# Kernel optimization log

Hardware: AMD Instinct MI355X
Metric: run time of the kernel (lower is better)

The kernel has to match this reference:

```python
import jax, jax.numpy as jnp
import numpy as np

B, N, C, G, H, DK = 8, 128, 128, 2, 4, 32
BN_SCALE = float(1.0 / np.sqrt(1.0 + 1e-5))  # eval-mode BatchNorm with running_mean=0, var=1, gamma=1, beta=0


def _l1norm(x):
    # F.normalize(p=1, dim=-1)
    return x / jnp.maximum(jnp.sum(jnp.abs(x), -1, keepdims=True), 1e-12)


def _bn(x):
    return x * BN_SCALE


def _lrelu(x):
    return jax.nn.leaky_relu(x, 0.01)


def setup_inputs() -> dict:
    key = jax.random.key(0)
    ks = jax.random.split(key, 14)
    p = lambda i, shape: jax.random.normal(ks[i], shape, jnp.float32) * 0.05
    return {
        "vp": jax.random.normal(ks[0], (B, N, C), jnp.float32),
        "ep0": jax.random.uniform(ks[1], (B, N, N), jnp.float32),
        # PointSimilarity_Pre 1x1-conv stack (stored as [in, out] matrices)
        "ps_pre_w1": p(2, (C, 2 * C)), "ps_pre_w2": p(3, (2 * C, C)),
        "ps_pre_w3": p(4, (C, 1)), "ps_pre_b3": jnp.zeros((1,), jnp.float32),
        # Per-generation PointSimilarity2 stacks
        "ps_w1": p(5, (G, C, 2 * C)), "ps_w2": p(6, (G, 2 * C, C)),
        "ps_w3": p(7, (G, C, 1)), "ps_b3": jnp.zeros((G, 1), jnp.float32),
        # Per-generation D2PAgg stacks (input is cat(vp, aggr) -> 2C channels)
        "d2p_w1": p(8, (G, 2 * C, 2 * C)), "d2p_w2": p(9, (G, 2 * C, C)),
        # Per-generation multi-head attention projections (d_model=C, n_head*d_k=C)
        "mha_wq": p(10, (G, C, H * DK)), "mha_wk": p(11, (G, C, H * DK)),
    }


def _psim(vp, ep_last, w1, w2, w3, b3, kval):
    # pairwise l2 distance features: [B, N, N, C]
    sim = (vp[:, :, None, :] - vp[:, None, :, :]) ** 2
    h = _lrelu(_bn(jnp.einsum('bijc,co->bijo', sim, w1)))
    h = _lrelu(_bn(jnp.einsum('bijc,co->bijo', h, w2)))
    e = jax.nn.sigmoid(jnp.einsum('bijc,co->bijo', h, w3)[..., 0] + b3)
    eye = jnp.eye(vp.shape[1], dtype=vp.dtype)
    ep_last = ep_last * (1.0 - eye)
    ep_sum = jnp.sum(ep_last, -1, keepdims=True)
    e = e * ep_last
    if kval is not None:  # neighbor attention via top-k sparsification
        _, idx = jax.lax.top_k(e, kval)
        b_i = jnp.arange(e.shape[0])[:, None, None]
        r_i = jnp.arange(e.shape[1])[None, :, None]
        mask = jnp.zeros_like(e).at[b_i, r_i, idx].set(1.0)
        e = e * mask
    e = _l1norm(e) * ep_sum
    e = e + eye + 1e-6
    e = e / jnp.sum(e, 2, keepdims=True)
    return e


def _d2p(ep, vp, w1, w2):
    eye = jnp.eye(vp.shape[1], dtype=vp.dtype)
    edge = _l1norm(ep * (1.0 - eye))
    aggr = jnp.einsum('bij,bjc->bic', edge, vp)  # bmm aggregation
    nf = jnp.concatenate([vp, aggr], -1)         # [B, N, 2C]
    h = _lrelu(_bn(nf @ w1))
    return _lrelu(_bn(h @ w2))


def _mha(vp, wq, wk):
    b, n, _ = vp.shape
    q = (vp @ wq).reshape(b, n, H, DK)
    k = (vp @ wk).reshape(b, n, H, DK)
    attn = jax.nn.softmax(jnp.einsum('bqhd,bkhd->bhqk', q, k) / np.sqrt(DK), axis=-1)
    return attn.mean(1)  # average heads -> [B, N, N]


def reference(vp, ep0, ps_pre_w1, ps_pre_w2, ps_pre_w3, ps_pre_b3,
              ps_w1, ps_w2, ps_w3, ps_b3, d2p_w1, d2p_w2, mha_wq, mha_wk):
    ep = _psim(vp, ep0, ps_pre_w1, ps_pre_w2, ps_pre_w3, ps_pre_b3, None)
    for g in range(G):
        attn = _mha(vp, mha_wq[g], mha_wk[g])
        vp = _d2p(ep * attn, vp, d2p_w1[g], d2p_w2[g])
        kval = int(N * (1.0 - 0.1 * (g + 1)))
        ep = _psim(vp, ep, ps_w1[g], ps_w2[g], ps_w3[g], ps_b3[g], kval)
    return ep
```

## Files before the change

### kernel.cpp

```cpp
#include <hip/hip_runtime.h>

typedef __bf16 bf16x8 __attribute__((ext_vector_type(8)));
typedef float floatx4 __attribute__((ext_vector_type(4)));

#define MFMA(a, b, c) __builtin_amdgcn_mfma_f32_16x16x32_bf16(a, b, c, 0, 0, 0)

#define BNS 0.9999950000374997f
#define LRELU(x) ((x) > 0.f ? (x) : 0.01f * (x))

__device__ inline float wave_sum(float v) {
#pragma unroll
  for (int s = 32; s > 0; s >>= 1) v += __shfl_xor(v, s, 64);
  return v;
}
__device__ inline float wave_max(float v) {
#pragma unroll
  for (int s = 32; s > 0; s >>= 1) v = fmaxf(v, __shfl_xor(v, s, 64));
  return v;
}

__global__ __launch_bounds__(256) void k_prep(const float* __restrict__ pre_w1,
                                              const float* __restrict__ ps_w1,
                                              const float* __restrict__ pre_w2,
                                              const float* __restrict__ ps_w2,
                                              const float* __restrict__ dw1,
                                              const float* __restrict__ dw2,
                                              const float* __restrict__ mwq,
                                              const float* __restrict__ mwk,
                                              __bf16* __restrict__ w1b,
                                              __bf16* __restrict__ w2b,
                                              __bf16* __restrict__ d1i,
                                              __bf16* __restrict__ d2i,
                                              __bf16* __restrict__ qki) {
  const int tt = blockIdx.x * 256 + threadIdx.x;
  bf16x8 v;
  if (tt < 24576) {
    const int buf = tt / 12288;
    const int r = tt % 12288;
    const int set = r >> 12;
    const int q = r & 4095;
    const int ln = q & 63, qd = ln >> 4, cc = ln & 15;
    const int wv = (q >> 6) & 3;
    if (buf == 0) {
      const int kt = (q >> 8) & 3, qtr = (q >> 10) & 3;
      const float* src = (set == 0) ? pre_w1 : ps_w1 + (size_t)(set - 1) * 32768;
      const float* p = src + (size_t)(kt * 32 + qd * 8) * 256 + qtr * 64 + wv * 16 + cc;
#pragma unroll
      for (int jj = 0; jj < 8; jj++) v[jj] = (__bf16)p[jj * 256];
      *(bf16x8*)&w1b[(size_t)set * 32768 + q * 8] = v;
    } else {
      const int kt = (q >> 8) & 1, nt = (q >> 9) & 1, qtr = (q >> 10) & 3;
      const float* src = (set == 0) ? pre_w2 : ps_w2 + (size_t)(set - 1) * 32768;
      const float* p = src + (size_t)(qtr * 64 + kt * 32 + qd * 8) * 128 + wv * 32 + nt * 16 + cc;
#pragma unroll
      for (int jj = 0; jj < 8; jj++) v[jj] = (__bf16)p[jj * 128];
      *(bf16x8*)&w2b[(size_t)set * 32768 + q * 8] = v;
    }
  } else if (tt < 40960) {
    const int u = tt - 24576;
    const int gen = u >> 13, r = u & 8191, cb = r >> 8, o = r & 255;
    const float* src = dw1 + (size_t)gen * 65536 + (size_t)(cb * 8) * 256 + o;
#pragma unroll
    for (int jj = 0; jj < 8; jj++) v[jj] = (__bf16)src[jj * 256];
    *(bf16x8*)&d1i[(size_t)(((gen * 32 + cb) * 256 + o)) * 8] = v;
  } else if (tt < 49152) {
    const int u = tt - 40960;
    const int gen = u >> 12, r = u & 4095, kb = r >> 7, o = r & 127;
    const float* src = dw2 + (size_t)gen * 32768 + (size_t)(kb * 8) * 128 + o;
#pragma unroll
    for (int jj = 0; jj < 8; jj++) v[jj] = (__bf16)src[jj * 128];
    *(bf16x8*)&d2i[(size_t)(((gen * 32 + kb) * 128 + o)) * 8] = v;
  } else if (tt < 57344) {
    const int u = tt - 49152;
    const int gen = u >> 12, r = u & 4095, qk = r >> 11, r2 = r & 2047;
    const int cb = r2 >> 7, o = r2 & 127;
    const float* src = (qk ? mwk : mwq) + (size_t)gen * 16384 + (size_t)(cb * 8) * 128 + o;
#pragma unroll
    for (int jj = 0; jj < 8; jj++) v[jj] = (__bf16)src[jj * 128];
    *(bf16x8*)&qki[(size_t)((((gen * 2 + qk) * 16 + cb) * 128 + o)) * 8] = v;
  }
}

__global__ void __launch_bounds__(256, 3)
k_psim(const float* __restrict__ vp, const float* __restrict__ ep_in,
       float* __restrict__ ep_out,
       const __bf16* __restrict__ w1b, const __bf16* __restrict__ w2b,
       const float* __restrict__ w3, const float* __restrict__ b3,
       int kval, float* __restrict__ outp) {
  __shared__ __bf16 simf[16384];
  __shared__ __bf16 hbf[8192];
  __shared__ float ep_row[128];
  __shared__ float e_row[128];
  __shared__ float w3s[128];
  __shared__ float red[256];
  __shared__ float red2[4];

  const int tid = threadIdx.x;
  const int b = blockIdx.x >> 7, i = blockIdx.x & 127;
  const float* vpb = vp + ((size_t)b << 14);
  const float* vpi = vpb + (i << 7);
  const size_t rowoff = ((size_t)blockIdx.x) << 7;

  {
    const int j = tid >> 1;
    const int c0 = (tid & 1) << 6;
    const int m = j >> 4, ccr = j & 15;
    const float* vpj = vpb + (j << 7) + c0;
    const float* vpx = vpi + c0;
#pragma unroll
    for (int c = 0; c < 64; c += 8) {
      const int gc = c0 + c;
      const int kt = gc >> 5, qdw = (gc >> 3) & 3;
      float4 a0 = *(const float4*)(vpj + c);
      float4 a1 = *(const float4*)(vpj + c + 4);
      float4 b0 = *(const float4*)(vpx + c);
      float4 b1 = *(const float4*)(vpx + c + 4);
      bf16x8 t;
      float d;
      d = a0.x - b0.x; t[0] = (__bf16)(d * d);
      d = a0.y - b0.y; t[1] = (__bf16)(d * d);
      d = a0.z - b0.z; t[2] = (__bf16)(d * d);
      d = a0.w - b0.w; t[3] = (__bf16)(d * d);
      d = a1.x - b1.x; t[4] = (__bf16)(d * d);
      d = a1.y - b1.y; t[5] = (__bf16)(d * d);
      d = a1.z - b1.z; t[6] = (__bf16)(d * d);
      d = a1.w - b1.w; t[7] = (__bf16)(d * d);
      *(bf16x8*)&simf[(((kt << 3) + m) << 6 | (qdw << 4 | ccr)) << 3] = t;
    }
    if (tid < 128) {
      ep_row[tid] = (tid == i) ? 0.f : ep_in[rowoff + tid];
      w3s[tid] = w3[tid];
    }
  }
  __syncthreads();

  const int wv = tid >> 6;
  const int ln = tid & 63;
  const int qd = ln >> 4;
  const int cc = ln & 15;

  floatx4 acc2[8][2];
#pragma unroll
  for (int m = 0; m < 8; m++) {
    acc2[m][0] = (floatx4){0.f, 0.f, 0.f, 0.f};
    acc2[m][1] = (floatx4){0.f, 0.f, 0.f, 0.f};
  }

  const int h1h = wv >> 1;
  const int h1qd = ((wv & 1) << 1) | (cc >> 3);
  const int h1jj = cc & 7;

  for (int qtr = 0; qtr < 4; qtr++) {
    bf16x8 bw[4];
#pragma unroll
    for (int kt = 0; kt < 4; kt++)
      bw[kt] = *(const bf16x8*)&w1b[((((qtr * 4 + kt) * 4 + wv) * 64) + ln) * 8];
#pragma unroll
    for (int m2 = 0; m2 < 8; m2 += 2) {
      bf16x8 af0[4], af1[4];
#pragma unroll
      for (int kt = 0; kt < 4; kt++) {
        af0[kt] = *(const bf16x8*)&simf[(((kt << 3) + m2) << 6 | ln) << 3];
        af1[kt] = *(const bf16x8*)&simf[(((kt << 3) + m2 + 1) << 6 | ln) << 3];
      }
      floatx4 x0 = (floatx4){0.f, 0.f, 0.f, 0.f};
      floatx4 x1 = (floatx4){0.f, 0.f, 0.f, 0.f};
#pragma unroll
      for (int kt = 0; kt < 4; kt++) {
        x0 = MFMA(af0[kt], bw[kt], x0);
        x1 = MFMA(af1[kt], bw[kt], x1);
      }
#pragma unroll
      for (int r = 0; r < 4; r++) {
        float v0 = x0[r] * BNS;
        float v1 = x1[r] * BNS;
        hbf[(((h1h * 8 + m2) * 64) + h1qd * 16 + qd * 4 + r) * 8 + h1jj] = (__bf16)LRELU(v0);
        hbf[(((h1h * 8 + m2 + 1) * 64) + h1qd * 16 + qd * 4 + r) * 8 + h1jj] = (__bf16)LRELU(v1);
      }
    }
    __syncthreads();

    bf16x8 bw2[2][2];
#pragma unroll
    for (int nt = 0; nt < 2; nt++)
#pragma unroll
      for (int kt = 0; kt < 2; kt++)
        bw2[nt][kt] = *(const bf16x8*)&w2b[(((((qtr * 2 + nt) * 2 + kt) * 4 + wv) * 64) + ln) * 8];
#pragma unroll
    for (int m = 0; m < 8; m++) {
      bf16x8 a0 = *(const bf16x8*)&hbf[((m << 6) | ln) << 3];
      bf16x8 a1 = *(const bf16x8*)&hbf[(((8 + m) << 6) | ln) << 3];
      acc2[m][0] = MFMA(a0, bw2[0][0], acc2[m][0]);
      acc2[m][1] = MFMA(a0, bw2[1][0], acc2[m][1]);
      acc2[m][0] = MFMA(a1, bw2[0][1], acc2[m][0]);
      acc2[m][1] = MFMA(a1, bw2[1][1], acc2[m][1]);
    }
    __syncthreads();
  }

  {
    const int seg = wv;
#pragma unroll
    for (int m = 0; m < 8; m++)
#pragma unroll
      for (int nt = 0; nt < 2; nt++) {
        const int q2 = (nt << 1) | (cc >> 3);
#pragma unroll
        for (int r = 0; r < 4; r++) {
          float v = acc2[m][nt][r] * BNS;
          simf[(((seg * 8 + m) * 64) + q2 * 16 + qd * 4 + r) * 8 + (cc & 7)] = (__bf16)LRELU(v);
        }
      }
  }
  __syncthreads();

  {
    const int j = tid & 127, hh = tid >> 7;
    const int m = j >> 4, R = j & 15;
    float s = 0.f;
#pragma unroll
    for (int sg = 0; sg < 2; sg++) {
      const int seg = hh * 2 + sg;
#pragma unroll
      for (int q3 = 0; q3 < 4; q3++) {
        bf16x8 f = *(const bf16x8*)&simf[(((seg * 8 + m) * 64) + q3 * 16 + R) * 8];
        const float* wp = &w3s[seg * 32 + q3 * 8];
#pragma unroll
        for (int jj = 0; jj < 8; jj++) s += (float)f[jj] * wp[jj];
      }
    }
    red[tid] = s;
  }
  __syncthreads();
  if (tid < 128) {
    float s = red[tid] + red[tid + 128] + b3[0];
    float sg = 1.f / (1.f + expf(-s));
    e_row[tid] = sg * ep_row[tid];
  }
  __syncthreads();

  {
    float v = (tid < 128) ? ep_row[tid] : 0.f;
    float w = wave_sum(v);
    if (ln == 0) red2[wv] = w;
  }
  __syncthreads();
  const float ep_sum = red2[0] + red2[1];

  if (kval > 0) {
    const int j = tid & 127, hh = tid >> 7;
    const float v = e_row[j];
    int cnt = 0;
    const int base = hh << 6;
#pragma unroll 8
    for (int jj = 0; jj < 64; jj++) {
      float u = e_row[base + jj];
      cnt += (u > v || (u == v && (base + jj) < j)) ? 1 : 0;
    }
    red[tid] = (float)cnt;
  }
  __syncthreads();

  float em = 0.f;
  if (tid < 128) {
    float v = e_row[tid];
    if (kval > 0) {
      int cnt = (int)red[tid] + (int)red[tid + 128];
      em = (cnt < kval) ? v : 0.f;
    } else {
      em = v;
    }
  }
  {
    float w = wave_sum((tid < 128) ? em : 0.f);
    if (ln == 0) red2[wv] = w;
  }
  __syncthreads();
  const float l1 = red2[0] + red2[1];
  __syncthreads();

  const float scale = ep_sum / fmaxf(l1, 1e-12f);
  float val = 0.f;
  if (tid < 128) val = em * scale + ((tid == i) ? 1.f : 0.f) + 1e-6f;
  {
    float w = wave_sum((tid < 128) ? val : 0.f);
    if (ln == 0) red2[wv] = w;
  }
  __syncthreads();
  const float rsum = red2[0] + red2[1];

  if (tid < 128) {
    float o = val / rsum;
    ep_out[rowoff + tid] = o;
    if (outp) outp[rowoff + tid] = o;
  }
}

__global__ __launch_bounds__(256) void k_qk(const float* __restrict__ vp,
                                            const __bf16* __restrict__ qkw,
                                            float* __restrict__ qo,
                                            float* __restrict__ ko) {
  __shared__ float vr[128];
  const int t = threadIdx.x;
  const size_t rowoff = ((size_t)blockIdx.x) << 7;
  if (t < 128) vr[t] = vp[rowoff + t];
  __syncthreads();
  const int o = t & 127;
  const __bf16* base = qkw + ((t >> 7) ? 16384 : 0);
  const float4* vr4 = (const float4*)vr;
  float a = 0.f;
#pragma unroll
  for (int cb = 0; cb < 16; cb++) {
    bf16x8 w8 = *(const bf16x8*)&base[(cb * 128 + o) * 8];
    float4 v0 = vr4[2 * cb], v1 = vr4[2 * cb + 1];
    a += v0.x * (float)w8[0] + v0.y * (float)w8[1] + v0.z * (float)w8[2] + v0.w * (float)w8[3] +
         v1.x * (float)w8[4] + v1.y * (float)w8[5] + v1.z * (float)w8[6] + v1.w * (float)w8[7];
  }
  float* dst = (t < 128) ? qo : ko;
  dst[rowoff + o] = a;
}

__global__ __launch_bounds__(256) void k_attn_d2p(const float* __restrict__ qv,
                                                  const float* __restrict__ kv,
                                                  const float* __restrict__ ep,
                                                  const float* __restrict__ vp_in,
                                                  const __bf16* __restrict__ d1,
                                                  const __bf16* __restrict__ d2,
                                                  float* __restrict__ vp_out) {
  __shared__ float qi[256];
  __shared__ float sbuf[1024];
  __shared__ float er[256];
  __shared__ float nf[512];
  __shared__ float hb[512];
  __shared__ float pbuf[2048];
  __shared__ float red2[4];

  const int tid = threadIdx.x;
  const int wv = tid >> 6, ln = tid & 63;
  const int b = blockIdx.x >> 6;
  const int r0 = (blockIdx.x & 63) * 2;
  const size_t rowoff0 = ((size_t)(b * 128 + r0)) << 7;
  const float* vpbb = vp_in + ((size_t)b << 14);

  qi[tid] = qv[rowoff0 + tid];
  __syncthreads();

  {
    const int j = tid & 127, hh = tid >> 7;
    const float* krow = kv + (((size_t)(b * 128 + j)) << 7);
    const int h0 = hh * 2, h1 = hh * 2 + 1;
    float s00 = 0.f, s01 = 0.f, s10 = 0.f, s11 = 0.f;
#pragma unroll
    for (int d = 0; d < 32; d += 4) {
      float4 k0 = *(const float4*)(krow + h0 * 32 + d);
      float4 k1 = *(const float4*)(krow + h1 * 32 + d);
      s00 += qi[h0 * 32 + d] * k0.x + qi[h0 * 32 + d + 1] * k0.y +
             qi[h0 * 32 + d + 2] * k0.z + qi[h0 * 32 + d + 3] * k0.w;
      s01 += qi[h1 * 32 + d] * k1.x + qi[h1 * 32 + d + 1] * k1.y +
             qi[h1 * 32 + d + 2] * k1.z + qi[h1 * 32 + d + 3] * k1.w;
      s10 += qi[128 + h0 * 32 + d] * k0.x + qi[128 + h0 * 32 + d + 1] * k0.y +
             qi[128 + h0 * 32 + d + 2] * k0.z + qi[128 + h0 * 32 + d + 3] * k0.w;
      s11 += qi[128 + h1 * 32 + d] * k1.x + qi[128 + h1 * 32 + d + 1] * k1.y +
             qi[128 + h1 * 32 + d + 2] * k1.z + qi[128 + h1 * 32 + d + 3] * k1.w;
    }
    const float sc = 0.17677669529663687f;
    sbuf[(0 * 4 + h0) * 128 + j] = s00 * sc;
    sbuf[(0 * 4 + h1) * 128 + j] = s01 * sc;
    sbuf[(1 * 4 + h0) * 128 + j] = s10 * sc;
    sbuf[(1 * 4 + h1) * 128 + j] = s11 * sc;
  }
  __syncthreads();

  {
    const int g = wv;
#pragma unroll
    for (int row = 0; row < 2; row++) {
      float a = sbuf[(row * 4 + g) * 128 + ln];
      float bb = sbuf[(row * 4 + g) * 128 + 64 + ln];
      float mx = wave_max(fmaxf(a, bb));
      float e0 = expf(a - mx), e1 = expf(bb - mx);
      float Z = wave_sum(e0 + e1);
      sbuf[(row * 4 + g) * 128 + ln] = e0 / Z;
      sbuf[(row * 4 + g) * 128 + 64 + ln] = e1 / Z;
    }
  }
  __syncthreads();

  {
    const int row = tid >> 7, j = tid & 127;
    float attn = 0.25f * (sbuf[(row * 4) * 128 + j] + sbuf[(row * 4 + 1) * 128 + j] +
                          sbuf[(row * 4 + 2) * 128 + j] + sbuf[(row * 4 + 3) * 128 + j]);
    float eraw = (j == r0 + row) ? 0.f : ep[rowoff0 + tid] * attn;
    float w = wave_sum(eraw);
    if (ln == 0) red2[wv] = w;
    __syncthreads();
    float l1row = red2[row * 2] + red2[row * 2 + 1];
    er[tid] = eraw / fmaxf(l1row, 1e-12f);
    nf[(row << 8) + j] = vp_in[rowoff0 + tid];
  }
  __syncthreads();

  {
    const int cg = tid & 31, jg = tid >> 5;
    float4 a0 = {0.f, 0.f, 0.f, 0.f}, a1 = {0.f, 0.f, 0.f, 0.f};
#pragma unroll
    for (int jj = 0; jj < 16; jj++) {
      const int j = jg * 16 + jj;
      float4 v = *(const float4*)(vpbb + (j << 7) + (cg << 2));
      float e0 = er[j], e1 = er[128 + j];
      a0.x += e0 * v.x; a0.y += e0 * v.y; a0.z += e0 * v.z; a0.w += e0 * v.w;
      a1.x += e1 * v.x; a1.y += e1 * v.y; a1.z += e1 * v.z; a1.w += e1 * v.w;
    }
    *(float4*)&pbuf[(jg * 32 + cg) * 4] = a0;
    *(float4*)&pbuf[1024 + (jg * 32 + cg) * 4] = a1;
  }
  __syncthreads();
  {
    const int row = tid >> 7, c = tid & 127;
    float s = 0.f;
#pragma unroll
    for (int jg = 0; jg < 8; jg++) s += pbuf[(row << 10) + jg * 128 + c];
    nf[(row << 8) + 128 + c] = s;
  }
  __syncthreads();

  {
    const int row = tid >> 7, o = tid & 127;
    const float4* nfr4 = (const float4*)&nf[row << 8];
    float a0 = 0.f, a1 = 0.f;
#pragma unroll 4
    for (int cb = 0; cb < 32; cb++) {
      bf16x8 wa = *(const bf16x8*)&d1[(cb * 256 + o) * 8];
      bf16x8 wb = *(const bf16x8*)&d1[(cb * 256 + o + 128) * 8];
      float4 n0 = nfr4[2 * cb], n1 = nfr4[2 * cb + 1];
      a0 += n0.x * (float)wa[0] + n0.y * (float)wa[1] + n0.z * (float)wa[2] + n0.w * (float)wa[3] +
            n1.x * (float)wa[4] + n1.y * (float)wa[5] + n1.z * (float)wa[6] + n1.w * (float)wa[7];
      a1 += n0.x * (float)wb[0] + n0.y * (float)wb[1] + n0.z * (float)wb[2] + n0.w * (float)wb[3] +
            n1.x * (float)wb[4] + n1.y * (float)wb[5] + n1.z * (float)wb[6] + n1.w * (float)wb[7];
    }
    hb[(row << 8) + o] = LRELU(a0 * BNS);
    hb[(row << 8) + o + 128] = LRELU(a1 * BNS);
  }
  __syncthreads();

  {
    const int row = tid >> 7, o = tid & 127;
    const float4* hbr4 = (const float4*)&hb[row << 8];
    float a = 0.f;
#pragma unroll 4
    for (int kb = 0; kb < 32; kb++) {
      bf16x8 w8 = *(const bf16x8*)&d2[(kb * 128 + o) * 8];
      float4 h0 = hbr4[2 * kb], h1 = hbr4[2 * kb + 1];
      a += h0.x * (float)w8[0] + h0.y * (float)w8[1] + h0.z * (float)w8[2] + h0.w * (float)w8[3] +
           h1.x * (float)w8[4] + h1.y * (float)w8[5] + h1.z * (float)w8[6] + h1.w * (float)w8[7];
    }
    vp_out[rowoff0 + tid] = LRELU(a * BNS);
  }
}

extern "C" void kernel_launch(void* const* d_in, const int* in_sizes, int n_in,
                              void* d_out, int out_size, void* d_ws, size_t ws_size,
                              hipStream_t stream) {
  const float* vp0    = (const float*)d_in[0];
  const float* ep0    = (const float*)d_in[1];
  const float* pre_w1 = (const float*)d_in[2];
  const float* pre_w2 = (const float*)d_in[3];
  const float* pre_w3 = (const float*)d_in[4];
  const float* pre_b3 = (const float*)d_in[5];
  const float* ps_w1  = (const float*)d_in[6];
  const float* ps_w2  = (const float*)d_in[7];
  const float* ps_w3  = (const float*)d_in[8];
  const float* ps_b3  = (const float*)d_in[9];
  const float* dw1    = (const float*)d_in[10];
  const float* dw2    = (const float*)d_in[11];
  const float* mwq    = (const float*)d_in[12];
  const float* mwk    = (const float*)d_in[13];

  char* ws = (char*)d_ws;
  float* ep   = (float*)(ws);
  float* vpb  = (float*)(ws + (512ull << 10));
  float* vpa  = (float*)(ws + (1024ull << 10));
  float* qf   = (float*)(ws + (1536ull << 10));
  float* kf   = (float*)(ws + (2048ull << 10));
  __bf16* w1b = (__bf16*)(ws + (2560ull << 10));
  __bf16* w2b = (__bf16*)(ws + (2560ull << 10) + 196608);
  __bf16* d1i = (__bf16*)(ws + (2560ull << 10) + 393216);
  __bf16* d2i = (__bf16*)(ws + (2560ull << 10) + 655360);
  __bf16* qki = (__bf16*)(ws + (2560ull << 10) + 786432);
  float* outp = (float*)d_out;

  k_prep<<<224, 256, 0, stream>>>(pre_w1, ps_w1, pre_w2, ps_w2, dw1, dw2, mwq, mwk,
                                  w1b, w2b, d1i, d2i, qki);

  k_psim<<<1024, 256, 0, stream>>>(vp0, ep0, ep, w1b, w2b, pre_w3, pre_b3, 0, nullptr);

  k_qk<<<1024, 256, 0, stream>>>(vp0, qki, qf, kf);
  k_attn_d2p<<<512, 256, 0, stream>>>(qf, kf, ep, vp0, d1i, d2i, vpb);
  k_psim<<<1024, 256, 0, stream>>>(vpb, ep, ep, w1b + 32768, w2b + 32768,
                                   ps_w3, ps_b3, 115, nullptr);

  k_qk<<<1024, 256, 0, stream>>>(vpb, qki + 32768, qf, kf);
  k_attn_d2p<<<512, 256, 0, stream>>>(qf, kf, ep, vpb, d1i + 65536, d2i + 32768, vpa);
  k_psim<<<1024, 256, 0, stream>>>(vpa, ep, ep, w1b + 65536, w2b + 65536,
                                   ps_w3 + 128, ps_b3 + 1, 102, outp);
}
```

Baseline: 231.3 us.

## Partition psim MLP by rows per wave, keeping features in registers

Restructures the pairwise-similarity MLP so each wave owns 32 neighbor rows and computes all output channels for them. The squared-difference features are built directly in registers, which removes the shared simf buffer. Per-wave hbf slices replace block-wide barriers inside the qtr loop. The final w3 projection is done from the accumulators with lane shuffles instead of a shared-memory round trip. This cuts LDS traffic and __syncthreads, at the cost of each wave loading all of w1/w2 and holding more accumulator registers, and the prep kernel's weight layouts are reordered to match.

```diff
diff --git a/kernel.cpp b/kernel.cpp
--- a/kernel.cpp
+++ b/kernel.cpp
@@ -40,18 +40,17 @@
     const int set = r >> 12;
     const int q = r & 4095;
     const int ln = q & 63, qd = ln >> 4, cc = ln & 15;
-    const int wv = (q >> 6) & 3;
     if (buf == 0) {
-      const int kt = (q >> 8) & 3, qtr = (q >> 10) & 3;
+      const int kt = (q >> 6) & 3, nt = (q >> 8) & 3, qtr = q >> 10;
       const float* src = (set == 0) ? pre_w1 : ps_w1 + (size_t)(set - 1) * 32768;
-      const float* p = src + (size_t)(kt * 32 + qd * 8) * 256 + qtr * 64 + wv * 16 + cc;
+      const float* p = src + (size_t)(kt * 32 + qd * 8) * 256 + qtr * 64 + nt * 16 + cc;
 #pragma unroll
       for (int jj = 0; jj < 8; jj++) v[jj] = (__bf16)p[jj * 256];
       *(bf16x8*)&w1b[(size_t)set * 32768 + q * 8] = v;
     } else {
-      const int kt = (q >> 8) & 1, nt = (q >> 9) & 1, qtr = (q >> 10) & 3;
+      const int kt = (q >> 6) & 1, ot = (q >> 7) & 7, qtr = q >> 10;
       const float* src = (set == 0) ? pre_w2 : ps_w2 + (size_t)(set - 1) * 32768;
-      const float* p = src + (size_t)(qtr * 64 + kt * 32 + qd * 8) * 128 + wv * 32 + nt * 16 + cc;
+      const float* p = src + (size_t)(qtr * 64 + kt * 32 + qd * 8) * 128 + ot * 16 + cc;
 #pragma unroll
       for (int jj = 0; jj < 8; jj++) v[jj] = (__bf16)p[jj * 128];
       *(bf16x8*)&w2b[(size_t)set * 32768 + q * 8] = v;
@@ -87,34 +86,39 @@
        const __bf16* __restrict__ w1b, const __bf16* __restrict__ w2b,
        const float* __restrict__ w3, const float* __restrict__ b3,
        int kval, float* __restrict__ outp) {
-  __shared__ __bf16 simf[16384];
   __shared__ __bf16 hbf[8192];
   __shared__ float ep_row[128];
   __shared__ float e_row[128];
+  __shared__ float pre_s[128];
   __shared__ float w3s[128];
   __shared__ float red[256];
   __shared__ float red2[4];
 
   const int tid = threadIdx.x;
+  const int wv = tid >> 6, ln = tid & 63;
+  const int qd = ln >> 4, cc = ln & 15;
   const int b = blockIdx.x >> 7, i = blockIdx.x & 127;
   const float* vpb = vp + ((size_t)b << 14);
   const float* vpi = vpb + (i << 7);
   const size_t rowoff = ((size_t)blockIdx.x) << 7;
 
-  {
-    const int j = tid >> 1;
-    const int c0 = (tid & 1) << 6;
-    const int m = j >> 4, ccr = j & 15;
-    const float* vpj = vpb + (j << 7) + c0;
-    const float* vpx = vpi + c0;
-#pragma unroll
-    for (int c = 0; c < 64; c += 8) {
-      const int gc = c0 + c;
-      const int kt = gc >> 5, qdw = (gc >> 3) & 3;
-      float4 a0 = *(const float4*)(vpj + c);
-      float4 a1 = *(const float4*)(vpj + c + 4);
-      float4 b0 = *(const float4*)(vpx + c);
-      float4 b1 = *(const float4*)(vpx + c + 4);
+  if (tid < 128) {
+    ep_row[tid] = (tid == i) ? 0.f : ep_in[rowoff + tid];
+    w3s[tid] = w3[tid];
+  }
+
+  bf16x8 af[2][4];
+#pragma unroll
+  for (int m2 = 0; m2 < 2; m2++) {
+    const int j = wv * 32 + m2 * 16 + cc;
+    const float* vpj = vpb + (j << 7);
+#pragma unroll
+    for (int kt = 0; kt < 4; kt++) {
+      const int c0 = kt * 32 + qd * 8;
+      float4 a0 = *(const float4*)(vpj + c0);
+      float4 a1 = *(const float4*)(vpj + c0 + 4);
+      float4 b0 = *(const float4*)(vpi + c0);
+      float4 b1 = *(const float4*)(vpi + c0 + 4);
       bf16x8 t;
       float d;
       d = a0.x - b0.x; t[0] = (__bf16)(d * d);
@@ -125,115 +129,80 @@
       d = a1.y - b1.y; t[5] = (__bf16)(d * d);
       d = a1.z - b1.z; t[6] = (__bf16)(d * d);
       d = a1.w - b1.w; t[7] = (__bf16)(d * d);
-      *(bf16x8*)&simf[(((kt << 3) + m) << 6 | (qdw << 4 | ccr)) << 3] = t;
-    }
-    if (tid < 128) {
-      ep_row[tid] = (tid == i) ? 0.f : ep_in[rowoff + tid];
-      w3s[tid] = w3[tid];
-    }
-  }
-  __syncthreads();
-
-  const int wv = tid >> 6;
-  const int ln = tid & 63;
-  const int qd = ln >> 4;
-  const int cc = ln & 15;
-
-  floatx4 acc2[8][2];
-#pragma unroll
-  for (int m = 0; m < 8; m++) {
-    acc2[m][0] = (floatx4){0.f, 0.f, 0.f, 0.f};
-    acc2[m][1] = (floatx4){0.f, 0.f, 0.f, 0.f};
-  }
-
-  const int h1h = wv >> 1;
-  const int h1qd = ((wv & 1) << 1) | (cc >> 3);
-  const int h1jj = cc & 7;
+      af[m2][kt] = t;
+    }
+  }
+
+  floatx4 acc2[2][8];
+#pragma unroll
+  for (int m2 = 0; m2 < 2; m2++)
+#pragma unroll
+    for (int ot = 0; ot < 8; ot++) acc2[m2][ot] = (floatx4){0.f, 0.f, 0.f, 0.f};
+
+  const int hbase = wv * 2048;
+  const int jj_s = cc & 7;
 
   for (int qtr = 0; qtr < 4; qtr++) {
-    bf16x8 bw[4];
-#pragma unroll
-    for (int kt = 0; kt < 4; kt++)
-      bw[kt] = *(const bf16x8*)&w1b[((((qtr * 4 + kt) * 4 + wv) * 64) + ln) * 8];
-#pragma unroll
-    for (int m2 = 0; m2 < 8; m2 += 2) {
-      bf16x8 af0[4], af1[4];
-#pragma unroll
-      for (int kt = 0; kt < 4; kt++) {
-        af0[kt] = *(const bf16x8*)&simf[(((kt << 3) + m2) << 6 | ln) << 3];
-        af1[kt] = *(const bf16x8*)&simf[(((kt << 3) + m2 + 1) << 6 | ln) << 3];
-      }
-      floatx4 x0 = (floatx4){0.f, 0.f, 0.f, 0.f};
-      floatx4 x1 = (floatx4){0.f, 0.f, 0.f, 0.f};
-#pragma unroll
-      for (int kt = 0; kt < 4; kt++) {
-        x0 = MFMA(af0[kt], bw[kt], x0);
-        x1 = MFMA(af1[kt], bw[kt], x1);
-      }
-#pragma unroll
-      for (int r = 0; r < 4; r++) {
-        float v0 = x0[r] * BNS;
-        float v1 = x1[r] * BNS;
-        hbf[(((h1h * 8 + m2) * 64) + h1qd * 16 + qd * 4 + r) * 8 + h1jj] = (__bf16)LRELU(v0);
-        hbf[(((h1h * 8 + m2 + 1) * 64) + h1qd * 16 + qd * 4 + r) * 8 + h1jj] = (__bf16)LRELU(v1);
-      }
-    }
-    __syncthreads();
-
-    bf16x8 bw2[2][2];
-#pragma unroll
-    for (int nt = 0; nt < 2; nt++)
-#pragma unroll
-      for (int kt = 0; kt < 2; kt++)
-        bw2[nt][kt] = *(const bf16x8*)&w2b[(((((qtr * 2 + nt) * 2 + kt) * 4 + wv) * 64) + ln) * 8];
-#pragma unroll
-    for (int m = 0; m < 8; m++) {
-      bf16x8 a0 = *(const bf16x8*)&hbf[((m << 6) | ln) << 3];
-      bf16x8 a1 = *(const bf16x8*)&hbf[(((8 + m) << 6) | ln) << 3];
-      acc2[m][0] = MFMA(a0, bw2[0][0], acc2[m][0]);
-      acc2[m][1] = MFMA(a0, bw2[1][0], acc2[m][1]);
-      acc2[m][0] = MFMA(a1, bw2[0][1], acc2[m][0]);
-      acc2[m][1] = MFMA(a1, bw2[1][1], acc2[m][1]);
-    }
-    __syncthreads();
-  }
-
-  {
-    const int seg = wv;
-#pragma unroll
-    for (int m = 0; m < 8; m++)
-#pragma unroll
-      for (int nt = 0; nt < 2; nt++) {
-        const int q2 = (nt << 1) | (cc >> 3);
+#pragma unroll
+    for (int nt = 0; nt < 4; nt++) {
+      bf16x8 bw[4];
+#pragma unroll
+      for (int kt = 0; kt < 4; kt++)
+        bw[kt] = *(const bf16x8*)&w1b[(size_t)(((qtr * 4 + nt) * 4 + kt) * 64 + ln) * 8];
+      const int kt2 = nt >> 1;
+      const int qd2 = ((nt << 1) | (cc >> 3)) & 3;
+#pragma unroll
+      for (int m2 = 0; m2 < 2; m2++) {
+        floatx4 x = (floatx4){0.f, 0.f, 0.f, 0.f};
+#pragma unroll
+        for (int kt = 0; kt < 4; kt++) x = MFMA(af[m2][kt], bw[kt], x);
+        const int base = hbase + ((kt2 * 2 + m2) * 64 + qd2 * 16) * 8 + jj_s;
 #pragma unroll
         for (int r = 0; r < 4; r++) {
-          float v = acc2[m][nt][r] * BNS;
-          simf[(((seg * 8 + m) * 64) + q2 * 16 + qd * 4 + r) * 8 + (cc & 7)] = (__bf16)LRELU(v);
+          float v = x[r] * BNS;
+          hbf[base + (qd * 4 + r) * 8] = (__bf16)LRELU(v);
         }
       }
-  }
-  __syncthreads();
-
-  {
-    const int j = tid & 127, hh = tid >> 7;
-    const int m = j >> 4, R = j & 15;
-    float s = 0.f;
-#pragma unroll
-    for (int sg = 0; sg < 2; sg++) {
-      const int seg = hh * 2 + sg;
-#pragma unroll
-      for (int q3 = 0; q3 < 4; q3++) {
-        bf16x8 f = *(const bf16x8*)&simf[(((seg * 8 + m) * 64) + q3 * 16 + R) * 8];
-        const float* wp = &w3s[seg * 32 + q3 * 8];
-#pragma unroll
-        for (int jj = 0; jj < 8; jj++) s += (float)f[jj] * wp[jj];
+    }
+    bf16x8 a2[2][2];
+#pragma unroll
+    for (int m2 = 0; m2 < 2; m2++)
+#pragma unroll
+      for (int kt = 0; kt < 2; kt++)
+        a2[m2][kt] = *(const bf16x8*)&hbf[hbase + ((kt * 2 + m2) * 64 + ln) * 8];
+#pragma unroll
+    for (int ot = 0; ot < 8; ot++) {
+      bf16x8 bo0 = *(const bf16x8*)&w2b[(size_t)(((qtr * 8 + ot) * 2 + 0) * 64 + ln) * 8];
+      bf16x8 bo1 = *(const bf16x8*)&w2b[(size_t)(((qtr * 8 + ot) * 2 + 1) * 64 + ln) * 8];
+#pragma unroll
+      for (int m2 = 0; m2 < 2; m2++) {
+        acc2[m2][ot] = MFMA(a2[m2][0], bo0, acc2[m2][ot]);
+        acc2[m2][ot] = MFMA(a2[m2][1], bo1, acc2[m2][ot]);
       }
     }
-    red[tid] = s;
+  }
+
+  __syncthreads();
+
+#pragma unroll
+  for (int m2 = 0; m2 < 2; m2++) {
+#pragma unroll
+    for (int r = 0; r < 4; r++) {
+      float p = 0.f;
+#pragma unroll
+      for (int ot = 0; ot < 8; ot++) {
+        float h = acc2[m2][ot][r] * BNS;
+        h = LRELU(h);
+        p += h * w3s[ot * 16 + cc];
+      }
+#pragma unroll
+      for (int mk = 1; mk < 16; mk <<= 1) p += __shfl_xor(p, mk, 64);
+      if (cc == 0) pre_s[wv * 32 + m2 * 16 + qd * 4 + r] = p;
+    }
   }
   __syncthreads();
   if (tid < 128) {
-    float s = red[tid] + red[tid + 128] + b3[0];
+    float s = pre_s[tid] + b3[0];
     float sg = 1.f / (1.f + expf(-s));
     e_row[tid] = sg * ep_row[tid];
   }
```

Result: slower. 242.1 us (+4.7%).

## Prefetch psim MFMA weights one quarter ahead and use one row per attn_d2p block

Applied to the files above, without the earlier changes.

In k_psim the bf16 weight fragments for the two MFMA stages are loaded one quarter-iteration ahead into registers, and the quarter loop is fully unrolled. This hides global weight-load latency behind the MFMA work. k_attn_d2p now handles one query row per block instead of two, launching 1024 blocks, which doubles parallelism and shrinks shared memory. The cost is extra register pressure in psim and more redundant reads of d1/d2 weights, since each block now covers half as many rows, and some threads sit idle in the reworked attention kernel.

```diff
diff --git a/kernel.cpp b/kernel.cpp
--- a/kernel.cpp
+++ b/kernel.cpp
@@ -101,6 +101,11 @@
   const float* vpi = vpb + (i << 7);
   const size_t rowoff = ((size_t)blockIdx.x) << 7;
 
+  const int wv = tid >> 6;
+  const int ln = tid & 63;
+  const int qd = ln >> 4;
+  const int cc = ln & 15;
+
   {
     const int j = tid >> 1;
     const int c0 = (tid & 1) << 6;
@@ -132,12 +137,18 @@
       w3s[tid] = w3[tid];
     }
   }
-  __syncthreads();
-
-  const int wv = tid >> 6;
-  const int ln = tid & 63;
-  const int qd = ln >> 4;
-  const int cc = ln & 15;
+
+  bf16x8 bw[4], bw2[2][2];
+#pragma unroll
+  for (int kt = 0; kt < 4; kt++)
+    bw[kt] = *(const bf16x8*)&w1b[(((0 * 4 + kt) * 4 + wv) * 64 + ln) * 8];
+#pragma unroll
+  for (int nt = 0; nt < 2; nt++)
+#pragma unroll
+    for (int kt = 0; kt < 2; kt++)
+      bw2[nt][kt] = *(const bf16x8*)&w2b[((((0 * 2 + nt) * 2 + kt) * 4 + wv) * 64 + ln) * 8];
+
+  __syncthreads();
 
   floatx4 acc2[8][2];
 #pragma unroll
@@ -150,11 +161,20 @@
   const int h1qd = ((wv & 1) << 1) | (cc >> 3);
   const int h1jj = cc & 7;
 
+#pragma unroll
   for (int qtr = 0; qtr < 4; qtr++) {
-    bf16x8 bw[4];
-#pragma unroll
-    for (int kt = 0; kt < 4; kt++)
-      bw[kt] = *(const bf16x8*)&w1b[((((qtr * 4 + kt) * 4 + wv) * 64) + ln) * 8];
+    bf16x8 bwn[4], bw2n[2][2];
+    if (qtr < 3) {
+#pragma unroll
+      for (int kt = 0; kt < 4; kt++)
+        bwn[kt] = *(const bf16x8*)&w1b[((((qtr + 1) * 4 + kt) * 4 + wv) * 64 + ln) * 8];
+#pragma unroll
+      for (int nt = 0; nt < 2; nt++)
+#pragma unroll
+        for (int kt = 0; kt < 2; kt++)
+          bw2n[nt][kt] = *(const bf16x8*)&w2b[(((((qtr + 1) * 2 + nt) * 2 + kt) * 4 + wv) * 64 + ln) * 8];
+    }
+
 #pragma unroll
     for (int m2 = 0; m2 < 8; m2 += 2) {
       bf16x8 af0[4], af1[4];
@@ -180,12 +200,6 @@
     }
     __syncthreads();
 
-    bf16x8 bw2[2][2];
-#pragma unroll
-    for (int nt = 0; nt < 2; nt++)
-#pragma unroll
-      for (int kt = 0; kt < 2; kt++)
-        bw2[nt][kt] = *(const bf16x8*)&w2b[(((((qtr * 2 + nt) * 2 + kt) * 4 + wv) * 64) + ln) * 8];
 #pragma unroll
     for (int m = 0; m < 8; m++) {
       bf16x8 a0 = *(const bf16x8*)&hbf[((m << 6) | ln) << 3];
@@ -196,6 +210,15 @@
       acc2[m][1] = MFMA(a1, bw2[1][1], acc2[m][1]);
     }
     __syncthreads();
+
+    if (qtr < 3) {
+#pragma unroll
+      for (int kt = 0; kt < 4; kt++) bw[kt] = bwn[kt];
+#pragma unroll
+      for (int nt = 0; nt < 2; nt++)
+#pragma unroll
+        for (int kt = 0; kt < 2; kt++) bw2[nt][kt] = bw2n[nt][kt];
+    }
   }
 
   {
@@ -327,125 +350,111 @@
                                                   const __bf16* __restrict__ d1,
                                                   const __bf16* __restrict__ d2,
                                                   float* __restrict__ vp_out) {
-  __shared__ float qi[256];
-  __shared__ float sbuf[1024];
-  __shared__ float er[256];
-  __shared__ float nf[512];
-  __shared__ float hb[512];
-  __shared__ float pbuf[2048];
+  __shared__ float qi[128];
+  __shared__ float sbuf[512];
+  __shared__ float er[128];
+  __shared__ float nf[256];
+  __shared__ float hb[256];
+  __shared__ float pbuf[1024];
   __shared__ float red2[4];
 
   const int tid = threadIdx.x;
   const int wv = tid >> 6, ln = tid & 63;
-  const int b = blockIdx.x >> 6;
-  const int r0 = (blockIdx.x & 63) * 2;
-  const size_t rowoff0 = ((size_t)(b * 128 + r0)) << 7;
+  const int b = blockIdx.x >> 7, i = blockIdx.x & 127;
+  const size_t rowoff = ((size_t)blockIdx.x) << 7;
   const float* vpbb = vp_in + ((size_t)b << 14);
 
-  qi[tid] = qv[rowoff0 + tid];
+  if (tid < 128) qi[tid] = qv[rowoff + tid];
   __syncthreads();
 
   {
     const int j = tid & 127, hh = tid >> 7;
     const float* krow = kv + (((size_t)(b * 128 + j)) << 7);
     const int h0 = hh * 2, h1 = hh * 2 + 1;
-    float s00 = 0.f, s01 = 0.f, s10 = 0.f, s11 = 0.f;
+    float s0 = 0.f, s1 = 0.f;
 #pragma unroll
     for (int d = 0; d < 32; d += 4) {
       float4 k0 = *(const float4*)(krow + h0 * 32 + d);
       float4 k1 = *(const float4*)(krow + h1 * 32 + d);
-      s00 += qi[h0 * 32 + d] * k0.x + qi[h0 * 32 + d + 1] * k0.y +
-             qi[h0 * 32 + d + 2] * k0.z + qi[h0 * 32 + d + 3] * k0.w;
-      s01 += qi[h1 * 32 + d] * k1.x + qi[h1 * 32 + d + 1] * k1.y +
-             qi[h1 * 32 + d + 2] * k1.z + qi[h1 * 32 + d + 3] * k1.w;
-      s10 += qi[128 + h0 * 32 + d] * k0.x + qi[128 + h0 * 32 + d + 1] * k0.y +
-             qi[128 + h0 * 32 + d + 2] * k0.z + qi[128 + h0 * 32 + d + 3] * k0.w;
-      s11 += qi[128 + h1 * 32 + d] * k1.x + qi[128 + h1 * 32 + d + 1] * k1.y +
-             qi[128 + h1 * 32 + d + 2] * k1.z + qi[128 + h1 * 32 + d + 3] * k1.w;
+      s0 += qi[h0 * 32 + d] * k0.x + qi[h0 * 32 + d + 1] * k0.y +
+            qi[h0 * 32 + d + 2] * k0.z + qi[h0 * 32 + d + 3] * k0.w;
+      s1 += qi[h1 * 32 + d] * k1.x + qi[h1 * 32 + d + 1] * k1.y +
+            qi[h1 * 32 + d + 2] * k1.z + qi[h1 * 32 + d + 3] * k1.w;
     }
     const float sc = 0.17677669529663687f;
-    sbuf[(0 * 4 + h0) * 128 + j] = s00 * sc;
-    sbuf[(0 * 4 + h1) * 128 + j] = s01 * sc;
-    sbuf[(1 * 4 + h0) * 128 + j] = s10 * sc;
-    sbuf[(1 * 4 + h1) * 128 + j] = s11 * sc;
+    sbuf[h0 * 128 + j] = s0 * sc;
+    sbuf[h1 * 128 + j] = s1 * sc;
   }
   __syncthreads();
 
   {
     const int g = wv;
-#pragma unroll
-    for (int row = 0; row < 2; row++) {
-      float a = sbuf[(row * 4 + g) * 128 + ln];
-      float bb = sbuf[(row * 4 + g) * 128 + 64 + ln];
-      float mx = wave_max(fmaxf(a, bb));
-      float e0 = expf(a - mx), e1 = expf(bb - mx);
-      float Z = wave_sum(e0 + e1);
-      sbuf[(row * 4 + g) * 128 + ln] = e0 / Z;
-      sbuf[(row * 4 + g) * 128 + 64 + ln] = e1 / Z;
-    }
-  }
-  __syncthreads();
-
-  {
-    const int row = tid >> 7, j = tid & 127;
-    float attn = 0.25f * (sbuf[(row * 4) * 128 + j] + sbuf[(row * 4 + 1) * 128 + j] +
-                          sbuf[(row * 4 + 2) * 128 + j] + sbuf[(row * 4 + 3) * 128 + j]);
-    float eraw = (j == r0 + row) ? 0.f : ep[rowoff0 + tid] * attn;
-    float w = wave_sum(eraw);
+    float a = sbuf[g * 128 + ln];
+    float bb = sbuf[g * 128 + 64 + ln];
+    float mx = wave_max(fmaxf(a, bb));
+    float e0 = expf(a - mx), e1 = expf(bb - mx);
+    float Z = wave_sum(e0 + e1);
+    sbuf[g * 128 + ln] = e0 / Z;
+    sbuf[g * 128 + 64 + ln] = e1 / Z;
+  }
+  __syncthreads();
+
+  float eraw = 0.f;
+  if (tid < 128) {
+    float attn = 0.25f * (sbuf[tid] + sbuf[128 + tid] + sbuf[256 + tid] + sbuf[384 + tid]);
+    eraw = (tid == i) ? 0.f : ep[rowoff + tid] * attn;
+  }
+  {
+    float w = wave_sum((tid < 128) ? eraw : 0.f);
     if (ln == 0) red2[wv] = w;
-    __syncthreads();
-    float l1row = red2[row * 2] + red2[row * 2 + 1];
-    er[tid] = eraw / fmaxf(l1row, 1e-12f);
-    nf[(row << 8) + j] = vp_in[rowoff0 + tid];
+  }
+  __syncthreads();
+  const float l1 = red2[0] + red2[1];
+  if (tid < 128) {
+    er[tid] = eraw / fmaxf(l1, 1e-12f);
+    nf[tid] = vp_in[rowoff + tid];
   }
   __syncthreads();
 
   {
     const int cg = tid & 31, jg = tid >> 5;
-    float4 a0 = {0.f, 0.f, 0.f, 0.f}, a1 = {0.f, 0.f, 0.f, 0.f};
+    float4 a0 = {0.f, 0.f, 0.f, 0.f};
 #pragma unroll
     for (int jj = 0; jj < 16; jj++) {
       const int j = jg * 16 + jj;
       float4 v = *(const float4*)(vpbb + (j << 7) + (cg << 2));
-      float e0 = er[j], e1 = er[128 + j];
+      float e0 = er[j];
       a0.x += e0 * v.x; a0.y += e0 * v.y; a0.z += e0 * v.z; a0.w += e0 * v.w;
-      a1.x += e1 * v.x; a1.y += e1 * v.y; a1.z += e1 * v.z; a1.w += e1 * v.w;
     }
     *(float4*)&pbuf[(jg * 32 + cg) * 4] = a0;
-    *(float4*)&pbuf[1024 + (jg * 32 + cg) * 4] = a1;
-  }
-  __syncthreads();
-  {
-    const int row = tid >> 7, c = tid & 127;
+  }
+  __syncthreads();
+  if (tid < 128) {
     float s = 0.f;
 #pragma unroll
-    for (int jg = 0; jg < 8; jg++) s += pbuf[(row << 10) + jg * 128 + c];
-    nf[(row << 8) + 128 + c] = s;
-  }
-  __syncthreads();
-
-  {
-    const int row = tid >> 7, o = tid & 127;
-    const float4* nfr4 = (const float4*)&nf[row << 8];
-    float a0 = 0.f, a1 = 0.f;
+    for (int jg = 0; jg < 8; jg++) s += pbuf[jg * 128 + tid];
+    nf[128 + tid] = s;
+  }
+  __syncthreads();
+
+  {
+    const int o = tid;
+    const float4* nfr4 = (const float4*)nf;
+    float a0 = 0.f;
 #pragma unroll 4
     for (int cb = 0; cb < 32; cb++) {
       bf16x8 wa = *(const bf16x8*)&d1[(cb * 256 + o) * 8];
-      bf16x8 wb = *(const bf16x8*)&d1[(cb * 256 + o + 128) * 8];
       float4 n0 = nfr4[2 * cb], n1 = nfr4[2 * cb + 1];
       a0 += n0.x * (float)wa[0] + n0.y * (float)wa[1] + n0.z * (float)wa[2] + n0.w * (float)wa[3] +
             n1.x * (float)wa[4] + n1.y * (float)wa[5] + n1.z * (float)wa[6] + n1.w * (float)wa[7];
-      a1 += n0.x * (float)wb[0] + n0.y * (float)wb[1] + n0.z * (float)wb[2] + n0.w * (float)wb[3] +
-            n1.x * (float)wb[4] + n1.y * (float)wb[5] + n1.z * (float)wb[6] + n1.w * (float)wb[7];
-    }
-    hb[(row << 8) + o] = LRELU(a0 * BNS);
-    hb[(row << 8) + o + 128] = LRELU(a1 * BNS);
-  }
-  __syncthreads();
-
-  {
-    const int row = tid >> 7, o = tid & 127;
-    const float4* hbr4 = (const float4*)&hb[row << 8];
+    }
+    hb[o] = LRELU(a0 * BNS);
+  }
+  __syncthreads();
+
+  if (tid < 128) {
+    const int o = tid;
+    const float4* hbr4 = (const float4*)hb;
     float a = 0.f;
 #pragma unroll 4
     for (int kb = 0; kb < 32; kb++) {
@@ -454,7 +463,7 @@
       a += h0.x * (float)w8[0] + h0.y * (float)w8[1] + h0.z * (float)w8[2] + h0.w * (float)w8[3] +
            h1.x * (float)w8[4] + h1.y * (float)w8[5] + h1.z * (float)w8[6] + h1.w * (float)w8[7];
     }
-    vp_out[rowoff0 + tid] = LRELU(a * BNS);
+    vp_out[rowoff + tid] = LRELU(a * BNS);
   }
 }
 
@@ -495,12 +504,12 @@
   k_psim<<<1024, 256, 0, stream>>>(vp0, ep0, ep, w1b, w2b, pre_w3, pre_b3, 0, nullptr);
 
   k_qk<<<1024, 256, 0, stream>>>(vp0, qki, qf, kf);
-  k_attn_d2p<<<512, 256, 0, stream>>>(qf, kf, ep, vp0, d1i, d2i, vpb);
+  k_attn_d2p<<<1024, 256, 0, stream>>>(qf, kf, ep, vp0, d1i, d2i, vpb);
   k_psim<<<1024, 256, 0, stream>>>(vpb, ep, ep, w1b + 32768, w2b + 32768,
                                    ps_w3, ps_b3, 115, nullptr);
 
   k_qk<<<1024, 256, 0, stream>>>(vpb, qki + 32768, qf, kf);
-  k_attn_d2p<<<512, 256, 0, stream>>>(qf, kf, ep, vpb, d1i + 65536, d2i + 32768, vpa);
+  k_attn_d2p<<<1024, 256, 0, stream>>>(qf, kf, ep, vpb, d1i + 65536, d2i + 32768, vpa);
   k_psim<<<1024, 256, 0, stream>>>(vpa, ep, ep, w1b + 65536, w2b + 65536,
                                    ps_w3 + 128, ps_b3 + 1, 102, outp);
 }
```

New measurement: 239.9 us. 1.04x slower.

## Split D2P MLP into separate MFMA kernel and prefetch psim weights across quarters

Applied to the files above, without the earlier changes.

The D2P MLP moves out of the attention-aggregation kernel into a new k_mlp kernel that runs the two layers on bf16 MFMA over 16-row tiles, replacing per-row scalar FMA loops. The d2p weight packing in k_prep is changed to match the MFMA fragment layout, and aggregation results go through a global buffer. In k_psim, the w1/w2 fragments for the next quarter are loaded one iteration ahead so global weight loads overlap MFMA work. The costs are two extra kernel launches, an extra global round trip for agg, lower precision for the MLP inputs, and more register pressure in psim.

```diff
diff --git a/kernel.cpp b/kernel.cpp
--- a/kernel.cpp
+++ b/kernel.cpp
@@ -58,18 +58,22 @@
     }
   } else if (tt < 40960) {
     const int u = tt - 24576;
-    const int gen = u >> 13, r = u & 8191, cb = r >> 8, o = r & 255;
-    const float* src = dw1 + (size_t)gen * 65536 + (size_t)(cb * 8) * 256 + o;
+    const int gen = u >> 13, r = u & 8191;
+    const int nt = r >> 9, kt = (r >> 6) & 7, ln = r & 63;
+    const int qd = ln >> 4, cc = ln & 15;
+    const float* src = dw1 + (size_t)gen * 65536 + (size_t)(kt * 32 + qd * 8) * 256 + nt * 16 + cc;
 #pragma unroll
     for (int jj = 0; jj < 8; jj++) v[jj] = (__bf16)src[jj * 256];
-    *(bf16x8*)&d1i[(size_t)(((gen * 32 + cb) * 256 + o)) * 8] = v;
+    *(bf16x8*)&d1i[((size_t)gen * 65536) + (size_t)r * 8] = v;
   } else if (tt < 49152) {
     const int u = tt - 40960;
-    const int gen = u >> 12, r = u & 4095, kb = r >> 7, o = r & 127;
-    const float* src = dw2 + (size_t)gen * 32768 + (size_t)(kb * 8) * 128 + o;
+    const int gen = u >> 12, r = u & 4095;
+    const int nt = r >> 9, kt = (r >> 6) & 7, ln = r & 63;
+    const int qd = ln >> 4, cc = ln & 15;
+    const float* src = dw2 + (size_t)gen * 32768 + (size_t)(kt * 32 + qd * 8) * 128 + nt * 16 + cc;
 #pragma unroll
     for (int jj = 0; jj < 8; jj++) v[jj] = (__bf16)src[jj * 128];
-    *(bf16x8*)&d2i[(size_t)(((gen * 32 + kb) * 128 + o)) * 8] = v;
+    *(bf16x8*)&d2i[((size_t)gen * 32768) + (size_t)r * 8] = v;
   } else if (tt < 57344) {
     const int u = tt - 49152;
     const int gen = u >> 12, r = u & 4095, qk = r >> 11, r2 = r & 2047;
@@ -100,6 +104,11 @@
   const float* vpb = vp + ((size_t)b << 14);
   const float* vpi = vpb + (i << 7);
   const size_t rowoff = ((size_t)blockIdx.x) << 7;
+
+  const int wv = tid >> 6;
+  const int ln = tid & 63;
+  const int qd = ln >> 4;
+  const int cc = ln & 15;
 
   {
     const int j = tid >> 1;
@@ -132,12 +141,18 @@
       w3s[tid] = w3[tid];
     }
   }
-  __syncthreads();
-
-  const int wv = tid >> 6;
-  const int ln = tid & 63;
-  const int qd = ln >> 4;
-  const int cc = ln & 15;
+
+  bf16x8 bw[4], bw2[2][2];
+#pragma unroll
+  for (int kt = 0; kt < 4; kt++)
+    bw[kt] = *(const bf16x8*)&w1b[(((0 * 4 + kt) * 4 + wv) * 64 + ln) * 8];
+#pragma unroll
+  for (int nt = 0; nt < 2; nt++)
+#pragma unroll
+    for (int kt = 0; kt < 2; kt++)
+      bw2[nt][kt] = *(const bf16x8*)&w2b[((((0 * 2 + nt) * 2 + kt) * 4 + wv) * 64 + ln) * 8];
+
+  __syncthreads();
 
   floatx4 acc2[8][2];
 #pragma unroll
@@ -150,11 +165,20 @@
   const int h1qd = ((wv & 1) << 1) | (cc >> 3);
   const int h1jj = cc & 7;
 
+#pragma unroll
   for (int qtr = 0; qtr < 4; qtr++) {
-    bf16x8 bw[4];
-#pragma unroll
-    for (int kt = 0; kt < 4; kt++)
-      bw[kt] = *(const bf16x8*)&w1b[((((qtr * 4 + kt) * 4 + wv) * 64) + ln) * 8];
+    bf16x8 bwn[4], bw2n[2][2];
+    if (qtr < 3) {
+#pragma unroll
+      for (int kt = 0; kt < 4; kt++)
+        bwn[kt] = *(const bf16x8*)&w1b[((((qtr + 1) * 4 + kt) * 4 + wv) * 64 + ln) * 8];
+#pragma unroll
+      for (int nt = 0; nt < 2; nt++)
+#pragma unroll
+        for (int kt = 0; kt < 2; kt++)
+          bw2n[nt][kt] = *(const bf16x8*)&w2b[(((((qtr + 1) * 2 + nt) * 2 + kt) * 4 + wv) * 64 + ln) * 8];
+    }
+
 #pragma unroll
     for (int m2 = 0; m2 < 8; m2 += 2) {
       bf16x8 af0[4], af1[4];
@@ -180,12 +204,6 @@
     }
     __syncthreads();
 
-    bf16x8 bw2[2][2];
-#pragma unroll
-    for (int nt = 0; nt < 2; nt++)
-#pragma unroll
-      for (int kt = 0; kt < 2; kt++)
-        bw2[nt][kt] = *(const bf16x8*)&w2b[(((((qtr * 2 + nt) * 2 + kt) * 4 + wv) * 64) + ln) * 8];
 #pragma unroll
     for (int m = 0; m < 8; m++) {
       bf16x8 a0 = *(const bf16x8*)&hbf[((m << 6) | ln) << 3];
@@ -196,6 +214,15 @@
       acc2[m][1] = MFMA(a1, bw2[1][1], acc2[m][1]);
     }
     __syncthreads();
+
+    if (qtr < 3) {
+#pragma unroll
+      for (int kt = 0; kt < 4; kt++) bw[kt] = bwn[kt];
+#pragma unroll
+      for (int nt = 0; nt < 2; nt++)
+#pragma unroll
+        for (int kt = 0; kt < 2; kt++) bw2[nt][kt] = bw2n[nt][kt];
+    }
   }
 
   {
@@ -320,18 +347,14 @@
   dst[rowoff + o] = a;
 }
 
-__global__ __launch_bounds__(256) void k_attn_d2p(const float* __restrict__ qv,
+__global__ __launch_bounds__(256) void k_attn_agg(const float* __restrict__ qv,
                                                   const float* __restrict__ kv,
                                                   const float* __restrict__ ep,
                                                   const float* __restrict__ vp_in,
-                                                  const __bf16* __restrict__ d1,
-                                                  const __bf16* __restrict__ d2,
-                                                  float* __restrict__ vp_out) {
+                                                  float* __restrict__ agg) {
   __shared__ float qi[256];
   __shared__ float sbuf[1024];
   __shared__ float er[256];
-  __shared__ float nf[512];
-  __shared__ float hb[512];
   __shared__ float pbuf[2048];
   __shared__ float red2[4];
 
@@ -396,7 +419,6 @@
     __syncthreads();
     float l1row = red2[row * 2] + red2[row * 2 + 1];
     er[tid] = eraw / fmaxf(l1row, 1e-12f);
-    nf[(row << 8) + j] = vp_in[rowoff0 + tid];
   }
   __syncthreads();
 
@@ -420,41 +442,80 @@
     float s = 0.f;
 #pragma unroll
     for (int jg = 0; jg < 8; jg++) s += pbuf[(row << 10) + jg * 128 + c];
-    nf[(row << 8) + 128 + c] = s;
-  }
-  __syncthreads();
-
-  {
-    const int row = tid >> 7, o = tid & 127;
-    const float4* nfr4 = (const float4*)&nf[row << 8];
-    float a0 = 0.f, a1 = 0.f;
-#pragma unroll 4
-    for (int cb = 0; cb < 32; cb++) {
-      bf16x8 wa = *(const bf16x8*)&d1[(cb * 256 + o) * 8];
-      bf16x8 wb = *(const bf16x8*)&d1[(cb * 256 + o + 128) * 8];
-      float4 n0 = nfr4[2 * cb], n1 = nfr4[2 * cb + 1];
-      a0 += n0.x * (float)wa[0] + n0.y * (float)wa[1] + n0.z * (float)wa[2] + n0.w * (float)wa[3] +
-            n1.x * (float)wa[4] + n1.y * (float)wa[5] + n1.z * (float)wa[6] + n1.w * (float)wa[7];
-      a1 += n0.x * (float)wb[0] + n0.y * (float)wb[1] + n0.z * (float)wb[2] + n0.w * (float)wb[3] +
-            n1.x * (float)wb[4] + n1.y * (float)wb[5] + n1.z * (float)wb[6] + n1.w * (float)wb[7];
-    }
-    hb[(row << 8) + o] = LRELU(a0 * BNS);
-    hb[(row << 8) + o + 128] = LRELU(a1 * BNS);
-  }
-  __syncthreads();
-
-  {
-    const int row = tid >> 7, o = tid & 127;
-    const float4* hbr4 = (const float4*)&hb[row << 8];
-    float a = 0.f;
-#pragma unroll 4
-    for (int kb = 0; kb < 32; kb++) {
-      bf16x8 w8 = *(const bf16x8*)&d2[(kb * 128 + o) * 8];
-      float4 h0 = hbr4[2 * kb], h1 = hbr4[2 * kb + 1];
-      a += h0.x * (float)w8[0] + h0.y * (float)w8[1] + h0.z * (float)w8[2] + h0.w * (float)w8[3] +
-           h1.x * (float)w8[4] + h1.y * (float)w8[5] + h1.z * (float)w8[6] + h1.w * (float)w8[7];
-    }
-    vp_out[rowoff0 + tid] = LRELU(a * BNS);
+    agg[rowoff0 + tid] = s;
+  }
+}
+
+__global__ __launch_bounds__(256) void k_mlp(const float* __restrict__ vp_in,
+                                             const float* __restrict__ agg,
+                                             const __bf16* __restrict__ d1,
+                                             const __bf16* __restrict__ d2,
+                                             float* __restrict__ vp_out) {
+  __shared__ __bf16 hls[4096];
+  const int tid = threadIdx.x;
+  const int wv = tid >> 6, ln = tid & 63, qd = ln >> 4, cc = ln & 15;
+  const int row = (blockIdx.x << 4) + cc;
+
+  bf16x8 af[8];
+#pragma unroll
+  for (int kt = 0; kt < 4; kt++) {
+    const float* p = vp_in + (size_t)row * 128 + kt * 32 + qd * 8;
+    float4 v0 = *(const float4*)p, v1 = *(const float4*)(p + 4);
+    bf16x8 t;
+    t[0] = (__bf16)v0.x; t[1] = (__bf16)v0.y; t[2] = (__bf16)v0.z; t[3] = (__bf16)v0.w;
+    t[4] = (__bf16)v1.x; t[5] = (__bf16)v1.y; t[6] = (__bf16)v1.z; t[7] = (__bf16)v1.w;
+    af[kt] = t;
+  }
+#pragma unroll
+  for (int kt = 0; kt < 4; kt++) {
+    const float* p = agg + (size_t)row * 128 + kt * 32 + qd * 8;
+    float4 v0 = *(const float4*)p, v1 = *(const float4*)(p + 4);
+    bf16x8 t;
+    t[0] = (__bf16)v0.x; t[1] = (__bf16)v0.y; t[2] = (__bf16)v0.z; t[3] = (__bf16)v0.w;
+    t[4] = (__bf16)v1.x; t[5] = (__bf16)v1.y; t[6] = (__bf16)v1.z; t[7] = (__bf16)v1.w;
+    af[4 + kt] = t;
+  }
+
+#pragma unroll
+  for (int nt = 0; nt < 4; nt++) {
+    const int ntg = wv * 4 + nt;
+    floatx4 acc = (floatx4){0.f, 0.f, 0.f, 0.f};
+#pragma unroll
+    for (int kt = 0; kt < 8; kt++) {
+      bf16x8 bw = *(const bf16x8*)&d1[((size_t)(ntg * 8 + kt) * 64 + ln) * 8];
+      acc = MFMA(af[kt], bw, acc);
+    }
+    const int col = ntg * 16 + cc;
+    const int kt2 = col >> 5, qd2 = (col >> 3) & 3, jjs = col & 7;
+#pragma unroll
+    for (int r = 0; r < 4; r++) {
+      float h = acc[r] * BNS;
+      const int m = qd * 4 + r;
+      hls[((kt2 * 64) + qd2 * 16 + m) * 8 + jjs] = (__bf16)LRELU(h);
+    }
+  }
+  __syncthreads();
+
+  bf16x8 a2[8];
+#pragma unroll
+  for (int kt2 = 0; kt2 < 8; kt2++)
+    a2[kt2] = *(const bf16x8*)&hls[(kt2 * 64 + ln) * 8];
+#pragma unroll
+  for (int nt = 0; nt < 2; nt++) {
+    const int ntg = wv * 2 + nt;
+    floatx4 o = (floatx4){0.f, 0.f, 0.f, 0.f};
+#pragma unroll
+    for (int kt2 = 0; kt2 < 8; kt2++) {
+      bf16x8 bw = *(const bf16x8*)&d2[((size_t)(ntg * 8 + kt2) * 64 + ln) * 8];
+      o = MFMA(a2[kt2], bw, o);
+    }
+    const int col = ntg * 16 + cc;
+#pragma unroll
+    for (int r = 0; r < 4; r++) {
+      float v = o[r] * BNS;
+      const int m = qd * 4 + r;
+      vp_out[(size_t)((blockIdx.x << 4) + m) * 128 + col] = LRELU(v);
+    }
   }
 }
 
@@ -487,6 +548,7 @@
   __bf16* d1i = (__bf16*)(ws + (2560ull << 10) + 393216);
   __bf16* d2i = (__bf16*)(ws + (2560ull << 10) + 655360);
   __bf16* qki = (__bf16*)(ws + (2560ull << 10) + 786432);
+  float* agg  = (float*)(ws + (2560ull << 10) + 917504);
   float* outp = (float*)d_out;
 
   k_prep<<<224, 256, 0, stream>>>(pre_w1, ps_w1, pre_w2, ps_w2, dw1, dw2, mwq, mwk,
@@ -495,12 +557,14 @@
   k_psim<<<1024, 256, 0, stream>>>(vp0, ep0, ep, w1b, w2b, pre_w3, pre_b3, 0, nullptr);
 
   k_qk<<<1024, 256, 0, stream>>>(vp0, qki, qf, kf);
-  k_attn_d2p<<<512, 256, 0, stream>>>(qf, kf, ep, vp0, d1i, d2i, vpb);
+  k_attn_agg<<<512, 256, 0, stream>>>(qf, kf, ep, vp0, agg);
+  k_mlp<<<64, 256, 0, stream>>>(vp0, agg, d1i, d2i, vpb);
   k_psim<<<1024, 256, 0, stream>>>(vpb, ep, ep, w1b + 32768, w2b + 32768,
                                    ps_w3, ps_b3, 115, nullptr);
 
   k_qk<<<1024, 256, 0, stream>>>(vpb, qki + 32768, qf, kf);
-  k_attn_d2p<<<512, 256, 0, stream>>>(qf, kf, ep, vpb, d1i + 65536, d2i + 32768, vpa);
+  k_attn_agg<<<512, 256, 0, stream>>>(qf, kf, ep, vpb, agg);
+  k_mlp<<<64, 256, 0, stream>>>(vpb, agg, d1i + 65536, d2i + 32768, vpa);
   k_psim<<<1024, 256, 0, stream>>>(vpa, ep, ep, w1b + 65536, w2b + 65536,
                                    ps_w3 + 128, ps_b3 + 1, 102, outp);
 }
```

Result: faster. 222.4 us (-3.9%).
